# Optimization experiments

Hardware: AMD Instinct MI355X
Metric: run time of the kernel (lower is better)

The kernel has to match this reference:

```python
import jax, jax.numpy as jnp
import numpy as np

J = 24
ROOT = 0
# SMPL kinematic tree parents
PARENTS = [-1, 0, 0, 0, 1, 2, 3, 4, 5, 6, 7, 8, 9, 9, 9, 12, 13, 14, 16, 17, 18, 19, 20, 21]
RES_SCALE = 0.1


def rodrigues(rvec):
    """Axis-angle (..., 3) -> rotation matrix (..., 3, 3)."""
    theta = jnp.linalg.norm(rvec, axis=-1, keepdims=True)          # (...,1)
    axis = rvec / jnp.maximum(theta, 1e-8)
    x, y, z = axis[..., 0], axis[..., 1], axis[..., 2]
    zero = jnp.zeros_like(x)
    K = jnp.stack([zero, -z, y, z, zero, -x, -y, x, zero], axis=-1)
    K = K.reshape(rvec.shape[:-1] + (3, 3))
    s = jnp.sin(theta)[..., None]
    c = jnp.cos(theta)[..., None]
    I = jnp.eye(3, dtype=rvec.dtype)
    return I + s * K + (1.0 - c) * (K @ K)


def _make_T(R, t):
    """(B,3,3),(B,3) -> (B,4,4) homogeneous transform."""
    B = R.shape[0]
    top = jnp.concatenate([R, t[..., None]], axis=-1)              # (B,3,4)
    bottom = jnp.broadcast_to(jnp.array([0., 0., 0., 1.], R.dtype), (B, 1, 4))
    return jnp.concatenate([top, bottom], axis=-2)


def calculate_kinematic(rest_pose, rvecs, root_locs):
    """rest_pose (J,3), rvecs (B,J,3), root_locs (B,3) -> kp (B,J,3), skts (B,J,4,4).
    Sequential tree-structured chain, unrolled over the 24 joints."""
    R = rodrigues(rvecs)                                           # (B,J,3,3)
    B = rvecs.shape[0]
    l2w = [None] * J
    l2w[ROOT] = _make_T(R[:, ROOT], root_locs)
    for j in range(1, J):
        p = PARENTS[j]
        t_local = jnp.broadcast_to(rest_pose[j] - rest_pose[p], (B, 3))
        l2w[j] = l2w[p] @ _make_T(R[:, j], t_local)
    l2w = jnp.stack(l2w, axis=1)                                   # (B,J,4,4)
    kp = l2w[..., :3, 3]                                           # (B,J,3)
    # skts = inverse(l2w) = [R^T, -R^T t]
    Rt = jnp.swapaxes(l2w[..., :3, :3], -1, -2)
    t_inv = -(Rt @ kp[..., None])                                  # (B,J,3,1)
    top = jnp.concatenate([Rt, t_inv], axis=-1)                    # (B,J,3,4)
    bottom = jnp.broadcast_to(jnp.array([0., 0., 0., 1.], l2w.dtype), (B, J, 1, 4))
    skts = jnp.concatenate([top, bottom], axis=-2)                 # (B,J,4,4)
    return kp, skts


def setup_inputs() -> dict:
    key = jax.random.key(0)
    ks = jax.random.split(key, 12)
    N, NU, E, W = 131072, 16384, 16, 128
    skip = N // NU
    din, dout = J * 3 + E, J * 3 + 3
    bones = jax.random.normal(ks[0], (N, J, 3), jnp.float32) * 0.2
    pelvis_buf = jax.random.normal(ks[1], (NU, 3), jnp.float32)
    kp_idxs = jnp.arange(N, dtype=jnp.int64) // skip
    rest_pose = jax.random.normal(ks[2], (J, 3), jnp.float32) * 0.3
    rest_pose = rest_pose.at[ROOT].set(0.0)
    # kp3d root must match pelvis buffer (original asserts allclose)
    kp3d = jnp.zeros((N, J, 3), jnp.float32).at[:, ROOT].set(pelvis_buf[kp_idxs])
    emb_table = jax.random.normal(ks[3], (NU, E), jnp.float32) * 0.02
    def lin(k, fan_in, fan_out):
        lim = 1.0 / np.sqrt(fan_in)
        k1, k2 = jax.random.split(k)
        return (jax.random.uniform(k1, (fan_in, fan_out), jnp.float32, -lim, lim),
                jax.random.uniform(k2, (fan_out,), jnp.float32, -lim, lim))
    W0, b0 = lin(ks[4], din, W)
    W1, b1 = lin(ks[5], W, W)
    W2, b2 = lin(ks[6], W, W)
    W3, b3 = lin(ks[7], W, dout)
    return dict(bones=bones, kp3d=kp3d, kp_idxs=kp_idxs, emb_table=emb_table,
                pelvis_buf=pelvis_buf, rest_pose=rest_pose,
                W0=W0, b0=b0, W1=W1, b1=b1, W2=W2, b2=b2, W3=W3, b3=b3,
                N_unique=NU)


def reference(bones, kp3d, kp_idxs, emb_table, pelvis_buf, rest_pose,
              W0, b0, W1, b1, W2, b2, W3, b3, N_unique):
    N = bones.shape[0]
    skip = N // N_unique
    rvecs = bones[::skip].reshape(N_unique, J * 3)                 # (Nu, 72)
    kp_u = kp_idxs[::skip]
    embs = emb_table[kp_u]                                         # (Nu, 16)
    pelvis = pelvis_buf[kp_u]                                      # (Nu, 3)
    x = jnp.concatenate([rvecs, embs], axis=-1)
    h = jax.nn.relu(x @ W0 + b0)
    h = jax.nn.relu(h @ W1 + b1)
    h = jax.nn.relu(h @ W2 + b2)
    residual = (h @ W3 + b3) * RES_SCALE                           # (Nu, 75)
    rvecs = (rvecs + residual[:, :J * 3]).reshape(N_unique, J, 3)
    pelvis = pelvis + residual[:, J * 3:]
    kp, skts = calculate_kinematic(rest_pose, rvecs, pelvis)
    # expand unique poses back to full batch ('i s ... -> (i s) ...')
    kp = jnp.repeat(kp, skip, axis=0)                              # (N,J,3)
    skts = jnp.repeat(skts, skip, axis=0)                          # (N,J,4,4)
    rvecs = jnp.repeat(rvecs, skip, axis=0)                        # (N,J,3)
    return kp, skts, rvecs
```

## Files before the change

### kernel.cpp

```cpp
#include <hip/hip_runtime.h>
#include <hip/hip_bf16.h>

typedef unsigned short u16;
using f32x4 = __attribute__((ext_vector_type(4))) float;
using s16x8 = __attribute__((ext_vector_type(8))) short;
using u32x4 = __attribute__((ext_vector_type(4))) unsigned int;

#define JNT 24
#define STRX 104
#define STRH 136

__device__ __forceinline__ u16 f2bf(float f) {
    unsigned int x; __builtin_memcpy(&x, &f, 4);
    unsigned int lsb = (x >> 16) & 1u;
    x += 0x7fffu + lsb;
    return (u16)(x >> 16);
}

__global__ void prep_weights(const float* __restrict__ W0, const float* __restrict__ W1,
                             const float* __restrict__ W2, const float* __restrict__ W3,
                             u16* __restrict__ wst) {
    int i = blockIdx.x * 256 + threadIdx.x;
    if (i < 12288) { int n = i / 96, k = i - n * 96; wst[i] = (k < 88) ? f2bf(W0[k * 128 + n]) : (u16)0; return; }
    i -= 12288;
    if (i < 16384) { int n = i >> 7, k = i & 127; wst[12288 + i] = f2bf(W1[k * 128 + n]); return; }
    i -= 16384;
    if (i < 16384) { int n = i >> 7, k = i & 127; wst[28672 + i] = f2bf(W2[k * 128 + n]); return; }
    i -= 16384;
    if (i < 10240) { int n = i >> 7, k = i & 127; wst[45056 + i] = (n < 75) ? f2bf(W3[k * 75 + n]) : (u16)0; }
}

template<int BASE, int CNT>
__device__ __forceinline__ void mlp_l3(const u16* __restrict__ H, const u16* __restrict__ W3t,
                                       const float* __restrict__ b3, float* __restrict__ res_s,
                                       int trow, int lr, int lk, int drow) {
    f32x4 acc[CNT];
#pragma unroll
    for (int t = 0; t < CNT; ++t) {
        int col = (BASE + t) * 16 + lr;
        float bv = (col < 75) ? b3[col] : 0.f;
        acc[t] = (f32x4){bv, bv, bv, bv};
    }
#pragma unroll
    for (int ks = 0; ks < 4; ++ks) {
        s16x8 a = *(const s16x8*)&H[(trow + lr) * STRH + ks * 32 + lk];
#pragma unroll
        for (int t = 0; t < CNT; ++t) {
            s16x8 b = *(const s16x8*)&W3t[((BASE + t) * 16 + lr) * 128 + ks * 32 + lk];
            acc[t] = __builtin_amdgcn_mfma_f32_16x16x32_bf16(a, b, acc[t], 0, 0, 0);
        }
    }
#pragma unroll
    for (int t = 0; t < CNT; ++t) {
        int col = (BASE + t) * 16 + lr;
        if (col < 75) {
#pragma unroll
            for (int q = 0; q < 4; ++q)
                res_s[(trow + drow + q) * 80 + col] = acc[t][q] * 0.1f;
        }
    }
}

__device__ const int KPARP[32] = {0,0,0,0,1,2,3,4,5,6,7,8,9,9,9,12,13,14,16,17,18,19,20,21,0,0,0,0,0,0,0,0};
__device__ const int KDEPP[32] = {0,1,1,1,2,2,2,3,3,3,4,4,4,4,4,5,5,5,6,6,7,7,8,8,99,99,99,99,99,99,99,99};

__global__ __launch_bounds__(256, 2)
void fused_kernel(const float* __restrict__ bones, const float* __restrict__ emb,
                  const float* __restrict__ pelvis, const float* __restrict__ rest,
                  const float* __restrict__ b0, const float* __restrict__ b1,
                  const float* __restrict__ b2, const float* __restrict__ b3,
                  const u16* __restrict__ wst, float* __restrict__ out,
                  int N, int bstride) {
    __shared__ __align__(16) unsigned char smem[34304];
    float* res_s = (float*)smem;
    u16* Xs = (u16*)(smem + 10240);
    u16* H1 = (u16*)(smem + 16896);
    u16* H2 = (u16*)(smem + 25600);
    float* so8 = (float*)(smem + 10240);

    const int tid = threadIdx.x;
    const int row0 = blockIdx.x * 32;

    for (int i = tid; i < 32 * 96; i += 256) {
        int r = i / 96, c = i - r * 96;
        int u = row0 + r;
        float v = 0.f;
        if (c < 72)      v = bones[(size_t)u * bstride + c];
        else if (c < 88) v = emb[(size_t)u * 16 + (c - 72)];
        Xs[r * STRX + c] = f2bf(v);
    }
    __syncthreads();

    const int lane = tid & 63;
    const int wave = tid >> 6;
    const int rt = wave >> 1;
    const int nh = wave & 1;
    const int trow = rt * 16;
    const int lr = lane & 15;
    const int lk = (lane >> 4) * 8;
    const int drow = (lane >> 4) * 4;
    const u16* W0t = wst;
    const u16* W1t = wst + 12288;
    const u16* W2t = wst + 28672;
    const u16* W3t = wst + 45056;

    {
        f32x4 acc[4];
#pragma unroll
        for (int t = 0; t < 4; ++t) { float bv = b0[(nh * 4 + t) * 16 + lr]; acc[t] = (f32x4){bv, bv, bv, bv}; }
#pragma unroll
        for (int ks = 0; ks < 3; ++ks) {
            s16x8 a = *(const s16x8*)&Xs[(trow + lr) * STRX + ks * 32 + lk];
#pragma unroll
            for (int t = 0; t < 4; ++t) {
                s16x8 b = *(const s16x8*)&W0t[((nh * 4 + t) * 16 + lr) * 96 + ks * 32 + lk];
                acc[t] = __builtin_amdgcn_mfma_f32_16x16x32_bf16(a, b, acc[t], 0, 0, 0);
            }
        }
#pragma unroll
        for (int t = 0; t < 4; ++t)
#pragma unroll
            for (int q = 0; q < 4; ++q)
                H1[(trow + drow + q) * STRH + (nh * 4 + t) * 16 + lr] = f2bf(fmaxf(acc[t][q], 0.f));
    }
    __syncthreads();
    {
        f32x4 acc[4];
#pragma unroll
        for (int t = 0; t < 4; ++t) { float bv = b1[(nh * 4 + t) * 16 + lr]; acc[t] = (f32x4){bv, bv, bv, bv}; }
#pragma unroll
        for (int ks = 0; ks < 4; ++ks) {
            s16x8 a = *(const s16x8*)&H1[(trow + lr) * STRH + ks * 32 + lk];
#pragma unroll
            for (int t = 0; t < 4; ++t) {
                s16x8 b = *(const s16x8*)&W1t[((nh * 4 + t) * 16 + lr) * 128 + ks * 32 + lk];
                acc[t] = __builtin_amdgcn_mfma_f32_16x16x32_bf16(a, b, acc[t], 0, 0, 0);
            }
        }
#pragma unroll
        for (int t = 0; t < 4; ++t)
#pragma unroll
            for (int q = 0; q < 4; ++q)
                H2[(trow + drow + q) * STRH + (nh * 4 + t) * 16 + lr] = f2bf(fmaxf(acc[t][q], 0.f));
    }
    __syncthreads();
    {
        f32x4 acc[4];
#pragma unroll
        for (int t = 0; t < 4; ++t) { float bv = b2[(nh * 4 + t) * 16 + lr]; acc[t] = (f32x4){bv, bv, bv, bv}; }
#pragma unroll
        for (int ks = 0; ks < 4; ++ks) {
            s16x8 a = *(const s16x8*)&H2[(trow + lr) * STRH + ks * 32 + lk];
#pragma unroll
            for (int t = 0; t < 4; ++t) {
                s16x8 b = *(const s16x8*)&W2t[((nh * 4 + t) * 16 + lr) * 128 + ks * 32 + lk];
                acc[t] = __builtin_amdgcn_mfma_f32_16x16x32_bf16(a, b, acc[t], 0, 0, 0);
            }
        }
        __syncthreads();
#pragma unroll
        for (int t = 0; t < 4; ++t)
#pragma unroll
            for (int q = 0; q < 4; ++q)
                H1[(trow + drow + q) * STRH + (nh * 4 + t) * 16 + lr] = f2bf(fmaxf(acc[t][q], 0.f));
    }
    __syncthreads();
    if (nh == 0) mlp_l3<0, 3>(H1, W3t, b3, res_s, trow, lr, lk, drow);
    else         mlp_l3<3, 2>(H1, W3t, b3, res_s, trow, lr, lk, drow);
    __syncthreads();

    const int half = lane >> 5, j = lane & 31;
    const int par = KPARP[j], dep = KDEPP[j];
    const int plane = (lane & 32) | par;

    const u32x4* ls = (const u32x4*)so8;
    u32x4* o4 = (u32x4*)out;
    const size_t r1 = (size_t)N * 18;
    const size_t r2 = (size_t)N * 114;

    for (int pass = 0; pass < 4; ++pass) {
        const int sloc8 = wave * 2 + half;
        const int sl = pass * 8 + sloc8;
        const size_t u = (size_t)row0 + sl;

        float R[3][3] = {{1.f,0.f,0.f},{0.f,1.f,0.f},{0.f,0.f,1.f}};
        float T[3] = {0.f, 0.f, 0.f};
        float rv0 = 0.f, rv1 = 0.f, rv2 = 0.f;

        if (j < JNT) {
            const float* rs = &res_s[sl * 80];
            const float* bn = &bones[u * (size_t)bstride];
            rv0 = bn[j * 3 + 0] + rs[j * 3 + 0];
            rv1 = bn[j * 3 + 1] + rs[j * 3 + 1];
            rv2 = bn[j * 3 + 2] + rs[j * 3 + 2];
            float th = sqrtf(rv0 * rv0 + rv1 * rv1 + rv2 * rv2);
            float s = sinf(th), c = cosf(th);
            float inv = 1.f / fmaxf(th, 1e-8f);
            float ax = rv0 * inv, ay = rv1 * inv, az = rv2 * inv;
            float K[3][3] = {{0.f, -az, ay}, {az, 0.f, -ax}, {-ay, ax, 0.f}};
            float KK[3][3];
#pragma unroll
            for (int r = 0; r < 3; ++r)
#pragma unroll
                for (int cc = 0; cc < 3; ++cc)
                    KK[r][cc] = K[r][0] * K[0][cc] + K[r][1] * K[1][cc] + K[r][2] * K[2][cc];
            float omc = 1.f - c;
#pragma unroll
            for (int r = 0; r < 3; ++r)
#pragma unroll
                for (int cc = 0; cc < 3; ++cc)
                    R[r][cc] = ((r == cc) ? 1.f : 0.f) + s * K[r][cc] + omc * KK[r][cc];
            if (j == 0) {
#pragma unroll
                for (int cc = 0; cc < 3; ++cc) T[cc] = pelvis[u * 3 + cc] + rs[72 + cc];
            } else {
#pragma unroll
                for (int cc = 0; cc < 3; ++cc) T[cc] = rest[j * 3 + cc] - rest[par * 3 + cc];
            }
        }

        for (int lev = 1; lev <= 8; ++lev) {
            float p00 = __shfl(R[0][0], plane), p01 = __shfl(R[0][1], plane), p02 = __shfl(R[0][2], plane);
            float p10 = __shfl(R[1][0], plane), p11 = __shfl(R[1][1], plane), p12 = __shfl(R[1][2], plane);
            float p20 = __shfl(R[2][0], plane), p21 = __shfl(R[2][1], plane), p22 = __shfl(R[2][2], plane);
            float q0  = __shfl(T[0],   plane), q1  = __shfl(T[1],   plane), q2  = __shfl(T[2],   plane);
            if (dep == lev) {
                float n00 = p00 * R[0][0] + p01 * R[1][0] + p02 * R[2][0];
                float n01 = p00 * R[0][1] + p01 * R[1][1] + p02 * R[2][1];
                float n02 = p00 * R[0][2] + p01 * R[1][2] + p02 * R[2][2];
                float n10 = p10 * R[0][0] + p11 * R[1][0] + p12 * R[2][0];
                float n11 = p10 * R[0][1] + p11 * R[1][1] + p12 * R[2][1];
                float n12 = p10 * R[0][2] + p11 * R[1][2] + p12 * R[2][2];
                float n20 = p20 * R[0][0] + p21 * R[1][0] + p22 * R[2][0];
                float n21 = p20 * R[0][1] + p21 * R[1][1] + p22 * R[2][1];
                float n22 = p20 * R[0][2] + p21 * R[1][2] + p22 * R[2][2];
                float m0  = p00 * T[0] + p01 * T[1] + p02 * T[2] + q0;
                float m1  = p10 * T[0] + p11 * T[1] + p12 * T[2] + q1;
                float m2  = p20 * T[0] + p21 * T[1] + p22 * T[2] + q2;
                R[0][0] = n00; R[0][1] = n01; R[0][2] = n02;
                R[1][0] = n10; R[1][1] = n11; R[1][2] = n12;
                R[2][0] = n20; R[2][1] = n21; R[2][2] = n22;
                T[0] = m0; T[1] = m1; T[2] = m2;
            }
        }

        if (j < JNT) {
            float* kp = &so8[sloc8 * 528 + j * 3];
            kp[0] = T[0]; kp[1] = T[1]; kp[2] = T[2];
            float* sk = &so8[sloc8 * 528 + 72 + j * 16];
#pragma unroll
            for (int r = 0; r < 3; ++r) {
                sk[r * 4 + 0] = R[0][r];
                sk[r * 4 + 1] = R[1][r];
                sk[r * 4 + 2] = R[2][r];
                sk[r * 4 + 3] = -(R[0][r] * T[0] + R[1][r] * T[1] + R[2][r] * T[2]);
            }
            sk[12] = 0.f; sk[13] = 0.f; sk[14] = 0.f; sk[15] = 1.0f;
            float* rv = &so8[sloc8 * 528 + 456 + j * 3];
            rv[0] = rv0; rv[1] = rv1; rv[2] = rv2;
        }
        __syncthreads();

        for (int i = tid; i < 8 * 1056; i += 256) {
            int s = i / 1056, w = i - s * 1056;
            size_t uu = (size_t)row0 + pass * 8 + s;
            const u32x4* src; size_t dst;
            if (w < 144)      { src = ls + s * 132 + (w % 18);              dst = uu * 144 + w; }
            else if (w < 912) { int w2 = w - 144;
                                src = ls + s * 132 + 18 + (w2 % 96);        dst = r1 + uu * 768 + w2; }
            else              { int w3 = w - 912;
                                src = ls + s * 132 + 114 + (w3 % 18);       dst = r2 + uu * 144 + w3; }
            o4[dst] = *src;
        }
        __syncthreads();
    }
}

extern "C" void kernel_launch(void* const* d_in, const int* in_sizes, int n_in,
                              void* d_out, int out_size, void* d_ws, size_t ws_size,
                              hipStream_t stream) {
    const float* bones  = (const float*)d_in[0];
    const float* emb    = (const float*)d_in[3];
    const float* pelvis = (const float*)d_in[4];
    const float* rest   = (const float*)d_in[5];
    const float* W0 = (const float*)d_in[6];
    const float* b0 = (const float*)d_in[7];
    const float* W1 = (const float*)d_in[8];
    const float* b1 = (const float*)d_in[9];
    const float* W2 = (const float*)d_in[10];
    const float* b2 = (const float*)d_in[11];
    const float* W3 = (const float*)d_in[12];
    const float* b3 = (const float*)d_in[13];

    const int N    = in_sizes[0] / 72;
    const int NU   = in_sizes[3] / 16;
    const int skip = N / NU;
    const int bstride = skip * 72;

    u16* wst = (u16*)d_ws;

    prep_weights<<<216, 256, 0, stream>>>(W0, W1, W2, W3, wst);
    fused_kernel<<<NU / 32, 256, 0, stream>>>(bones, emb, pelvis, rest,
                                              b0, b1, b2, b3, wst,
                                              (float*)d_out, N, bstride);
}
```

Before: 76.04 us.

## Double-buffer kinematic output staging to overlap stores with next pass compute

```diff
diff --git a/kernel.cpp b/kernel.cpp
--- a/kernel.cpp
+++ b/kernel.cpp
@@ -64,19 +64,20 @@
 __device__ const int KPARP[32] = {0,0,0,0,1,2,3,4,5,6,7,8,9,9,9,12,13,14,16,17,18,19,20,21,0,0,0,0,0,0,0,0};
 __device__ const int KDEPP[32] = {0,1,1,1,2,2,2,3,3,3,4,4,4,4,4,5,5,5,6,6,7,7,8,8,99,99,99,99,99,99,99,99};
 
-__global__ __launch_bounds__(256, 2)
+__global__ __launch_bounds__(256, 3)
 void fused_kernel(const float* __restrict__ bones, const float* __restrict__ emb,
                   const float* __restrict__ pelvis, const float* __restrict__ rest,
                   const float* __restrict__ b0, const float* __restrict__ b1,
                   const float* __restrict__ b2, const float* __restrict__ b3,
                   const u16* __restrict__ wst, float* __restrict__ out,
                   int N, int bstride) {
-    __shared__ __align__(16) unsigned char smem[34304];
+    __shared__ __align__(16) unsigned char smem[44032];
     float* res_s = (float*)smem;
     u16* Xs = (u16*)(smem + 10240);
     u16* H1 = (u16*)(smem + 16896);
     u16* H2 = (u16*)(smem + 25600);
-    float* so8 = (float*)(smem + 10240);
+    float* bufA = (float*)(smem + 10240);
+    float* bufB = (float*)(smem + 27136);
 
     const int tid = threadIdx.x;
     const int row0 = blockIdx.x * 32;
@@ -173,12 +174,28 @@
     const int par = KPARP[j], dep = KDEPP[j];
     const int plane = (lane & 32) | par;
 
-    const u32x4* ls = (const u32x4*)so8;
     u32x4* o4 = (u32x4*)out;
     const size_t r1 = (size_t)N * 18;
     const size_t r2 = (size_t)N * 114;
 
+#define WRITE_PASS(wp, buf)                                                            \
+    {                                                                                  \
+        const u32x4* ls = (const u32x4*)(buf);                                         \
+        for (int i = tid; i < 8 * 1056; i += 256) {                                    \
+            int s = i / 1056, w = i - s * 1056;                                        \
+            size_t uu = (size_t)row0 + (wp) * 8 + s;                                   \
+            const u32x4* src; size_t dst;                                              \
+            if (w < 144)      { src = ls + s * 132 + (w % 18);        dst = uu * 144 + w; }            \
+            else if (w < 912) { int w2 = w - 144;                                      \
+                                src = ls + s * 132 + 18 + (w2 % 96);  dst = r1 + uu * 768 + w2; }      \
+            else              { int w3 = w - 912;                                      \
+                                src = ls + s * 132 + 114 + (w3 % 18); dst = r2 + uu * 144 + w3; }      \
+            o4[dst] = *src;                                                            \
+        }                                                                              \
+    }
+
     for (int pass = 0; pass < 4; ++pass) {
+        float* sbuf = (pass & 1) ? bufB : bufA;
         const int sloc8 = wave * 2 + half;
         const int sl = pass * 8 + sloc8;
         const size_t u = (size_t)row0 + sl;
@@ -244,10 +261,12 @@
             }
         }
 
+        __syncthreads();
+
         if (j < JNT) {
-            float* kp = &so8[sloc8 * 528 + j * 3];
+            float* kp = &sbuf[sloc8 * 528 + j * 3];
             kp[0] = T[0]; kp[1] = T[1]; kp[2] = T[2];
-            float* sk = &so8[sloc8 * 528 + 72 + j * 16];
+            float* sk = &sbuf[sloc8 * 528 + 72 + j * 16];
 #pragma unroll
             for (int r = 0; r < 3; ++r) {
                 sk[r * 4 + 0] = R[0][r];
@@ -256,24 +275,18 @@
                 sk[r * 4 + 3] = -(R[0][r] * T[0] + R[1][r] * T[1] + R[2][r] * T[2]);
             }
             sk[12] = 0.f; sk[13] = 0.f; sk[14] = 0.f; sk[15] = 1.0f;
-            float* rv = &so8[sloc8 * 528 + 456 + j * 3];
+            float* rv = &sbuf[sloc8 * 528 + 456 + j * 3];
             rv[0] = rv0; rv[1] = rv1; rv[2] = rv2;
         }
         __syncthreads();
 
-        for (int i = tid; i < 8 * 1056; i += 256) {
-            int s = i / 1056, w = i - s * 1056;
-            size_t uu = (size_t)row0 + pass * 8 + s;
-            const u32x4* src; size_t dst;
-            if (w < 144)      { src = ls + s * 132 + (w % 18);              dst = uu * 144 + w; }
-            else if (w < 912) { int w2 = w - 144;
-                                src = ls + s * 132 + 18 + (w2 % 96);        dst = r1 + uu * 768 + w2; }
-            else              { int w3 = w - 912;
-                                src = ls + s * 132 + 114 + (w3 % 18);       dst = r2 + uu * 144 + w3; }
-            o4[dst] = *src;
-        }
-        __syncthreads();
-    }
+        if (pass >= 1) {
+            float* wbuf = ((pass - 1) & 1) ? bufB : bufA;
+            WRITE_PASS(pass - 1, wbuf);
+        }
+    }
+    WRITE_PASS(3, bufB);
+#undef WRITE_PASS
 }
 
 extern "C" void kernel_launch(void* const* d_in, const int* in_sizes, int n_in,
```

Result: slower. 78.59 us (+3.4%).

## Halve rows per block to 16 and split MLP columns across four waves

Applied to the files above, without the earlier changes.

```diff
diff --git a/kernel.cpp b/kernel.cpp
--- a/kernel.cpp
+++ b/kernel.cpp
@@ -33,7 +33,7 @@
 template<int BASE, int CNT>
 __device__ __forceinline__ void mlp_l3(const u16* __restrict__ H, const u16* __restrict__ W3t,
                                        const float* __restrict__ b3, float* __restrict__ res_s,
-                                       int trow, int lr, int lk, int drow) {
+                                       int lr, int lk, int drow) {
     f32x4 acc[CNT];
 #pragma unroll
     for (int t = 0; t < CNT; ++t) {
@@ -43,7 +43,7 @@
     }
 #pragma unroll
     for (int ks = 0; ks < 4; ++ks) {
-        s16x8 a = *(const s16x8*)&H[(trow + lr) * STRH + ks * 32 + lk];
+        s16x8 a = *(const s16x8*)&H[lr * STRH + ks * 32 + lk];
 #pragma unroll
         for (int t = 0; t < CNT; ++t) {
             s16x8 b = *(const s16x8*)&W3t[((BASE + t) * 16 + lr) * 128 + ks * 32 + lk];
@@ -56,7 +56,7 @@
         if (col < 75) {
 #pragma unroll
             for (int q = 0; q < 4; ++q)
-                res_s[(trow + drow + q) * 80 + col] = acc[t][q] * 0.1f;
+                res_s[(drow + q) * 80 + col] = acc[t][q] * 0.1f;
         }
     }
 }
@@ -64,24 +64,24 @@
 __device__ const int KPARP[32] = {0,0,0,0,1,2,3,4,5,6,7,8,9,9,9,12,13,14,16,17,18,19,20,21,0,0,0,0,0,0,0,0};
 __device__ const int KDEPP[32] = {0,1,1,1,2,2,2,3,3,3,4,4,4,4,4,5,5,5,6,6,7,7,8,8,99,99,99,99,99,99,99,99};
 
-__global__ __launch_bounds__(256, 2)
+__global__ __launch_bounds__(256, 3)
 void fused_kernel(const float* __restrict__ bones, const float* __restrict__ emb,
                   const float* __restrict__ pelvis, const float* __restrict__ rest,
                   const float* __restrict__ b0, const float* __restrict__ b1,
                   const float* __restrict__ b2, const float* __restrict__ b3,
                   const u16* __restrict__ wst, float* __restrict__ out,
                   int N, int bstride) {
-    __shared__ __align__(16) unsigned char smem[34304];
+    __shared__ __align__(16) unsigned char smem[22016];
     float* res_s = (float*)smem;
-    u16* Xs = (u16*)(smem + 10240);
-    u16* H1 = (u16*)(smem + 16896);
-    u16* H2 = (u16*)(smem + 25600);
-    float* so8 = (float*)(smem + 10240);
+    u16* Xs = (u16*)(smem + 5120);
+    u16* H1 = (u16*)(smem + 8448);
+    u16* H2 = (u16*)(smem + 12800);
+    float* so8 = (float*)(smem + 5120);
 
     const int tid = threadIdx.x;
-    const int row0 = blockIdx.x * 32;
-
-    for (int i = tid; i < 32 * 96; i += 256) {
+    const int row0 = blockIdx.x * 16;
+
+    for (int i = tid; i < 16 * 96; i += 256) {
         int r = i / 96, c = i - r * 96;
         int u = row0 + r;
         float v = 0.f;
@@ -93,9 +93,6 @@
 
     const int lane = tid & 63;
     const int wave = tid >> 6;
-    const int rt = wave >> 1;
-    const int nh = wave & 1;
-    const int trow = rt * 16;
     const int lr = lane & 15;
     const int lk = (lane >> 4) * 8;
     const int drow = (lane >> 4) * 4;
@@ -105,68 +102,70 @@
     const u16* W3t = wst + 45056;
 
     {
-        f32x4 acc[4];
-#pragma unroll
-        for (int t = 0; t < 4; ++t) { float bv = b0[(nh * 4 + t) * 16 + lr]; acc[t] = (f32x4){bv, bv, bv, bv}; }
+        f32x4 acc[2];
+#pragma unroll
+        for (int t = 0; t < 2; ++t) { float bv = b0[(wave * 2 + t) * 16 + lr]; acc[t] = (f32x4){bv, bv, bv, bv}; }
 #pragma unroll
         for (int ks = 0; ks < 3; ++ks) {
-            s16x8 a = *(const s16x8*)&Xs[(trow + lr) * STRX + ks * 32 + lk];
-#pragma unroll
-            for (int t = 0; t < 4; ++t) {
-                s16x8 b = *(const s16x8*)&W0t[((nh * 4 + t) * 16 + lr) * 96 + ks * 32 + lk];
+            s16x8 a = *(const s16x8*)&Xs[lr * STRX + ks * 32 + lk];
+#pragma unroll
+            for (int t = 0; t < 2; ++t) {
+                s16x8 b = *(const s16x8*)&W0t[((wave * 2 + t) * 16 + lr) * 96 + ks * 32 + lk];
                 acc[t] = __builtin_amdgcn_mfma_f32_16x16x32_bf16(a, b, acc[t], 0, 0, 0);
             }
         }
 #pragma unroll
-        for (int t = 0; t < 4; ++t)
+        for (int t = 0; t < 2; ++t)
 #pragma unroll
             for (int q = 0; q < 4; ++q)
-                H1[(trow + drow + q) * STRH + (nh * 4 + t) * 16 + lr] = f2bf(fmaxf(acc[t][q], 0.f));
+                H1[(drow + q) * STRH + (wave * 2 + t) * 16 + lr] = f2bf(fmaxf(acc[t][q], 0.f));
     }
     __syncthreads();
     {
-        f32x4 acc[4];
-#pragma unroll
-        for (int t = 0; t < 4; ++t) { float bv = b1[(nh * 4 + t) * 16 + lr]; acc[t] = (f32x4){bv, bv, bv, bv}; }
+        f32x4 acc[2];
+#pragma unroll
+        for (int t = 0; t < 2; ++t) { float bv = b1[(wave * 2 + t) * 16 + lr]; acc[t] = (f32x4){bv, bv, bv, bv}; }
 #pragma unroll
         for (int ks = 0; ks < 4; ++ks) {
-            s16x8 a = *(const s16x8*)&H1[(trow + lr) * STRH + ks * 32 + lk];
-#pragma unroll
-            for (int t = 0; t < 4; ++t) {
-                s16x8 b = *(const s16x8*)&W1t[((nh * 4 + t) * 16 + lr) * 128 + ks * 32 + lk];
+            s16x8 a = *(const s16x8*)&H1[lr * STRH + ks * 32 + lk];
+#pragma unroll
+            for (int t = 0; t < 2; ++t) {
+                s16x8 b = *(const s16x8*)&W1t[((wave * 2 + t) * 16 + lr) * 128 + ks * 32 + lk];
                 acc[t] = __builtin_amdgcn_mfma_f32_16x16x32_bf16(a, b, acc[t], 0, 0, 0);
             }
         }
 #pragma unroll
-        for (int t = 0; t < 4; ++t)
+        for (int t = 0; t < 2; ++t)
 #pragma unroll
             for (int q = 0; q < 4; ++q)
-                H2[(trow + drow + q) * STRH + (nh * 4 + t) * 16 + lr] = f2bf(fmaxf(acc[t][q], 0.f));
+                H2[(drow + q) * STRH + (wave * 2 + t) * 16 + lr] = f2bf(fmaxf(acc[t][q], 0.f));
     }
     __syncthreads();
     {
-        f32x4 acc[4];
-#pragma unroll
-        for (int t = 0; t < 4; ++t) { float bv = b2[(nh * 4 + t) * 16 + lr]; acc[t] = (f32x4){bv, bv, bv, bv}; }
+        f32x4 acc[2];
+#pragma unroll
+        for (int t = 0; t < 2; ++t) { float bv = b2[(wave * 2 + t) * 16 + lr]; acc[t] = (f32x4){bv, bv, bv, bv}; }
 #pragma unroll
         for (int ks = 0; ks < 4; ++ks) {
-            s16x8 a = *(const s16x8*)&H2[(trow + lr) * STRH + ks * 32 + lk];
-#pragma unroll
-            for (int t = 0; t < 4; ++t) {
-                s16x8 b = *(const s16x8*)&W2t[((nh * 4 + t) * 16 + lr) * 128 + ks * 32 + lk];
+            s16x8 a = *(const s16x8*)&H2[lr * STRH + ks * 32 + lk];
+#pragma unroll
+            for (int t = 0; t < 2; ++t) {
+                s16x8 b = *(const s16x8*)&W2t[((wave * 2 + t) * 16 + lr) * 128 + ks * 32 + lk];
                 acc[t] = __builtin_amdgcn_mfma_f32_16x16x32_bf16(a, b, acc[t], 0, 0, 0);
             }
         }
         __syncthreads();
 #pragma unroll
-        for (int t = 0; t < 4; ++t)
+        for (int t = 0; t < 2; ++t)
 #pragma unroll
             for (int q = 0; q < 4; ++q)
-                H1[(trow + drow + q) * STRH + (nh * 4 + t) * 16 + lr] = f2bf(fmaxf(acc[t][q], 0.f));
-    }
-    __syncthreads();
-    if (nh == 0) mlp_l3<0, 3>(H1, W3t, b3, res_s, trow, lr, lk, drow);
-    else         mlp_l3<3, 2>(H1, W3t, b3, res_s, trow, lr, lk, drow);
+                H1[(drow + q) * STRH + (wave * 2 + t) * 16 + lr] = f2bf(fmaxf(acc[t][q], 0.f));
+    }
+    __syncthreads();
+    if      (wave == 0) mlp_l3<0, 2>(H1, W3t, b3, res_s, lr, lk, drow);
+    else if (wave == 1) mlp_l3<2, 1>(H1, W3t, b3, res_s, lr, lk, drow);
+    else if (wave == 2) mlp_l3<3, 1>(H1, W3t, b3, res_s, lr, lk, drow);
+    else                mlp_l3<4, 1>(H1, W3t, b3, res_s, lr, lk, drow);
     __syncthreads();
 
     const int half = lane >> 5, j = lane & 31;
@@ -178,7 +177,7 @@
     const size_t r1 = (size_t)N * 18;
     const size_t r2 = (size_t)N * 114;
 
-    for (int pass = 0; pass < 4; ++pass) {
+    for (int pass = 0; pass < 2; ++pass) {
         const int sloc8 = wave * 2 + half;
         const int sl = pass * 8 + sloc8;
         const size_t u = (size_t)row0 + sl;
@@ -300,7 +299,7 @@
     u16* wst = (u16*)d_ws;
 
     prep_weights<<<216, 256, 0, stream>>>(W0, W1, W2, W3, wst);
-    fused_kernel<<<NU / 32, 256, 0, stream>>>(bones, emb, pelvis, rest,
+    fused_kernel<<<NU / 16, 256, 0, stream>>>(bones, emb, pelvis, rest,
                                               b0, b1, b2, b3, wst,
                                               (float*)d_out, N, bstride);
 }
```

Measured after the change: 70.73 us. 7.0% less time.
